# Optimization experiments

Hardware: AMD Instinct MI355X
Metric: run time of the kernel (lower is better)

## Reference

```python
import jax, jax.numpy as jnp
import numpy as np

MS_KS = 9
C = 256
BN_EPS = 1e-5


def setup_inputs() -> dict:
    key = jax.random.key(0)
    k1, k2, k3 = jax.random.split(key, 3)
    p2_r = jax.random.normal(k1, (2, C, 64, 128), dtype=jnp.float32)
    conv_w = jax.random.normal(k2, (C, C, 1, MS_KS), dtype=jnp.float32) * 0.02
    conv1_w = jax.random.normal(k3, (1, C, 1, 1), dtype=jnp.float32) * 0.05
    bn_gamma = jnp.ones((1,), jnp.float32)
    bn_beta = jnp.zeros((1,), jnp.float32)
    return dict(p2_r=p2_r, conv_w=conv_w, conv1_w=conv1_w,
                bn_gamma=bn_gamma, bn_beta=bn_beta)


def _scnn_pass(x, M):
    # x: [b,c,h,w]. Each step applies conv(1,ms_ks) to a width-1 column with
    # zero padding ms_ks//2 -> only the center tap contributes, i.e. a 256x256
    # channel matmul per column, followed by relu and residual add.
    cols = jnp.moveaxis(x, 3, 0)  # [w,b,c,h]
    def step(carry, col):
        new = col + jax.nn.relu(jnp.einsum('oc,bch->boh', M, carry))
        return new, new
    _, outs = jax.lax.scan(step, cols[0], cols[1:])
    outs = jnp.concatenate([cols[:1], outs], axis=0)[::-1]  # mirrors out[::-1]
    return jnp.moveaxis(outs, 0, 3)


def _upsample_bilinear_ac(x, factor=4):
    # F.interpolate(mode='bilinear', align_corners=True)
    b, c, h, w = x.shape
    Ho, Wo = factor * h, factor * w
    ys = jnp.arange(Ho, dtype=x.dtype) * ((h - 1) / (Ho - 1))
    xs = jnp.arange(Wo, dtype=x.dtype) * ((w - 1) / (Wo - 1))
    y0 = jnp.floor(ys).astype(jnp.int32)
    y1 = jnp.minimum(y0 + 1, h - 1)
    wy = (ys - y0.astype(x.dtype))[None, None, :, None]
    rows = x[:, :, y0, :] * (1 - wy) + x[:, :, y1, :] * wy  # [b,c,Ho,w]
    x0 = jnp.floor(xs).astype(jnp.int32)
    x1 = jnp.minimum(x0 + 1, w - 1)
    wx = (xs - x0.astype(x.dtype))[None, None, None, :]
    return rows[:, :, :, x0] * (1 - wx) + rows[:, :, :, x1] * wx


def reference(p2_r, conv_w, conv1_w, bn_gamma, bn_beta):
    M = conv_w[:, :, 0, MS_KS // 2]  # center tap, [c_out, c_in]
    x = _scnn_pass(p2_r, M)                     # reverse=False
    x = _scnn_pass(x[:, :, :, ::-1], M)         # reverse=True (slices[::-1])
    x = _upsample_bilinear_ac(x, 4)             # [b,256,4h,4w]
    x = jnp.einsum('oc,bchw->bohw', conv1_w[:, :, 0, 0], x)  # 1x1 conv -> 1 ch
    # BatchNorm2d(1), training-mode batch statistics (biased variance)
    mean = jnp.mean(x, axis=(0, 2, 3), keepdims=True)
    var = jnp.mean((x - mean) ** 2, axis=(0, 2, 3), keepdims=True)
    x = (x - mean) * jax.lax.rsqrt(var + BN_EPS)
    x = x * bn_gamma[None, :, None, None] + bn_beta[None, :, None, None]
    return jax.nn.sigmoid(x)
```

## Files before the change

kernel.cpp:

```cpp
#include <hip/hip_runtime.h>


typedef _Float16 f16x8 __attribute__((ext_vector_type(8)));
typedef _Float16 f16x4 __attribute__((ext_vector_type(4)));
typedef float    f32x4 __attribute__((ext_vector_type(4)));

static __device__ __forceinline__ void sync_lds() {
  asm volatile("s_waitcnt lgkmcnt(0)" ::: "memory");
  __builtin_amdgcn_s_barrier();
  asm volatile("" ::: "memory");
}

static __device__ __forceinline__ float dpp_even(float v) {
  int t = __builtin_bit_cast(int, v);
  t = __builtin_amdgcn_update_dpp(t, t, 0xA0, 0xF, 0xF, false);
  return __builtin_bit_cast(float, t);
}

extern "C" __global__ void k_extract(const float* __restrict__ convw,
                                     _Float16* __restrict__ Md) {
  int q = blockIdx.x * 256 + threadIdx.x;
  float4 v = ((const float4*)convw)[q];
  float vv[4] = {v.x, v.y, v.z, v.w};
  int f = q * 4;
#pragma unroll
  for (int e = 0; e < 4; ++e) {
    int flat = f + e;
    if (flat % 9 == 4) Md[flat / 9] = (_Float16)vv[e];
  }
}

struct SM {
  _Float16 cy[2][256];
  _Float16 pad_[32];
  _Float16 zh[128 * 256];
};

extern "C" __global__ void __launch_bounds__(512, 1)
k_scan(const float* __restrict__ p2, const _Float16* __restrict__ Md,
       const float* __restrict__ conv1, float* __restrict__ sout,
       float* __restrict__ stats) {
  __shared__ SM sm;
  const int tid  = threadIdx.x;
  const int l    = tid & 63;
  const int r    = tid >> 6;
  const int col  = l & 15;
  const int quad = l >> 4;
  const int b    = blockIdx.x >> 6;
  const int h    = blockIdx.x & 63;

  if (blockIdx.x == 0 && tid == 0) { stats[0] = 0.f; stats[1] = 0.f; }

  const bool isY   = (col == 0);
  const bool isZ   = (col == 1);
  const bool zlane = (l & 1);

  const int m0 = (r * 2 + 0) * 16 + quad * 4;
  const int m1 = (r * 2 + 1) * 16 + quad * 4;

  f16x8 A0[8], A1[8];
#pragma unroll
  for (int ch = 0; ch < 8; ++ch) {
    A0[ch] = *(const f16x8*)(Md + ((r*2+0)*16 + col) * 256 + ch*32 + quad*8);
    A1[ch] = *(const f16x8*)(Md + ((r*2+1)*16 + col) * 256 + ch*32 + quad*8);
  }

  const float* pbase = p2 + (size_t)b * 2097152 + (size_t)h * 128;

  float4 pA[4], pB[4], qA[4], qB[4];
  if (isY) {
#pragma unroll
    for (int i = 0; i < 4; ++i) {
      pA[i] = *(const float4*)(pbase + (size_t)(m0 + i) * 8192);
      pB[i] = *(const float4*)(pbase + (size_t)(m1 + i) * 8192);
      qA[i] = *(const float4*)(pbase + (size_t)(m0 + i) * 8192 + 4);
      qB[i] = *(const float4*)(pbase + (size_t)(m1 + i) * 8192 + 4);
    }
  }

  if (isY) {
    f16x4 pa, pb;
#pragma unroll
    for (int i = 0; i < 4; ++i) {
      pa[i] = (_Float16)pA[i].x; pb[i] = (_Float16)pB[i].x;
    }
    *(f16x4*)(sm.cy[0] + m0) = pa; *(f16x4*)(sm.cy[0] + m1) = pb;
    *(f16x4*)(sm.zh    + m0) = pa; *(f16x4*)(sm.zh    + m1) = pb;
  }
  sync_lds();

  const _Float16* pY0 = sm.cy[0] + quad * 8;
  const _Float16* pY1 = sm.cy[1] + quad * 8;
  const _Float16* zrd = sm.zh + quad * 8;
  _Float16*       zwr = sm.zh + 256;

#define STEP(PY, WY, CA, CB, COMP)                                             \
  do {                                                                         \
    const _Float16* bsrc = zlane ? zrd : (PY);                                 \
    f16x8 B[8];                                                                \
    _Pragma("unroll")                                                          \
    for (int ch = 0; ch < 8; ++ch)                                             \
      B[ch] = *(const f16x8*)(bsrc + ch * 32);                                 \
    f32x4 a00 = {0.f,0.f,0.f,0.f}, a01 = {0.f,0.f,0.f,0.f};                    \
    f32x4 a10 = {0.f,0.f,0.f,0.f}, a11 = {0.f,0.f,0.f,0.f};                    \
    _Pragma("unroll")                                                          \
    for (int ch = 0; ch < 4; ++ch) {                                           \
      a00 = __builtin_amdgcn_mfma_f32_16x16x32_f16(A0[ch],   B[ch],   a00,0,0,0);\
      a10 = __builtin_amdgcn_mfma_f32_16x16x32_f16(A1[ch],   B[ch],   a10,0,0,0);\
      a01 = __builtin_amdgcn_mfma_f32_16x16x32_f16(A0[ch+4], B[ch+4], a01,0,0,0);\
      a11 = __builtin_amdgcn_mfma_f32_16x16x32_f16(A1[ch+4], B[ch+4], a11,0,0,0);\
    }                                                                          \
    f32x4 acc0 = a00 + a01, acc1 = a10 + a11;                                  \
    f32x4 yf0 = {}, yf1 = {};                                                  \
    if (isY) {                                                                 \
      f16x4 yh0, yh1;                                                          \
      _Pragma("unroll")                                                        \
      for (int i = 0; i < 4; ++i) {                                            \
        yf0[i] = (CA)[i].COMP + fmaxf(acc0[i], 0.f);                           \
        yf1[i] = (CB)[i].COMP + fmaxf(acc1[i], 0.f);                           \
        yh0[i] = (_Float16)yf0[i]; yh1[i] = (_Float16)yf1[i];                  \
      }                                                                        \
      *(f16x4*)((WY) + m0) = yh0;                                              \
      *(f16x4*)((WY) + m1) = yh1;                                              \
    }                                                                          \
    _Pragma("unroll")                                                          \
    for (int i = 0; i < 4; ++i) {                                              \
      yf0[i] = dpp_even(yf0[i]);                                               \
      yf1[i] = dpp_even(yf1[i]);                                               \
    }                                                                          \
    if (isZ) {                                                                 \
      f16x4 zh0, zh1;                                                          \
      _Pragma("unroll")                                                        \
      for (int i = 0; i < 4; ++i) {                                            \
        zh0[i] = (_Float16)(yf0[i] + fmaxf(acc0[i], 0.f));                     \
        zh1[i] = (_Float16)(yf1[i] + fmaxf(acc1[i], 0.f));                     \
      }                                                                        \
      *(f16x4*)(zwr + m0) = zh0;                                               \
      *(f16x4*)(zwr + m1) = zh1;                                               \
    }                                                                          \
    zrd += 256; zwr += 256;                                                    \
    sync_lds();                                                                \
  } while (0)

#define REFILL(SA, SB, W0)                                                     \
  do {                                                                         \
    if (isY) {                                                                 \
      int wt = (W0) <= 124 ? (W0) : 124;                                       \
      _Pragma("unroll")                                                        \
      for (int i = 0; i < 4; ++i) {                                            \
        SA[i] = *(const float4*)(pbase + (size_t)(m0 + i) * 8192 + wt);        \
        SB[i] = *(const float4*)(pbase + (size_t)(m1 + i) * 8192 + wt);        \
      }                                                                        \
    }                                                                          \
  } while (0)

  STEP(pY0, sm.cy[1], pA, pB, y);
  STEP(pY1, sm.cy[0], pA, pB, z);
  STEP(pY0, sm.cy[1], pA, pB, w);
  REFILL(pA, pB, 8);

  int w0 = 4;
#pragma unroll 1
  for (int it = 0; it < 15; ++it) {
    STEP(pY1, sm.cy[0], qA, qB, x);
    STEP(pY0, sm.cy[1], qA, qB, y);
    STEP(pY1, sm.cy[0], qA, qB, z);
    STEP(pY0, sm.cy[1], qA, qB, w);
    REFILL(qA, qB, w0 + 8);
    STEP(pY1, sm.cy[0], pA, pB, x);
    STEP(pY0, sm.cy[1], pA, pB, y);
    STEP(pY1, sm.cy[0], pA, pB, z);
    STEP(pY0, sm.cy[1], pA, pB, w);
    REFILL(pA, pB, w0 + 12);
    w0 += 8;
  }

  STEP(pY1, sm.cy[0], qA, qB, x);
  STEP(pY0, sm.cy[1], qA, qB, y);
  STEP(pY1, sm.cy[0], qA, qB, z);
  STEP(pY0, sm.cy[1], qA, qB, w);
#undef STEP
#undef REFILL

  {
    const int w    = tid >> 2;
    const int part = tid & 3;
    const _Float16* zr = sm.zh + w * 256 + part * 64;
    const float*    vr = conv1 + part * 64;
    float s = 0.f;
#pragma unroll
    for (int j = 0; j < 8; ++j) {
      f16x8 zv = *(const f16x8*)(zr + j * 8);
      float4 v0 = *(const float4*)(vr + j * 8);
      float4 v1 = *(const float4*)(vr + j * 8 + 4);
      s += v0.x * (float)zv[0] + v0.y * (float)zv[1]
         + v0.z * (float)zv[2] + v0.w * (float)zv[3]
         + v1.x * (float)zv[4] + v1.y * (float)zv[5]
         + v1.z * (float)zv[6] + v1.w * (float)zv[7];
    }
    s += __shfl_xor(s, 1, 64);
    s += __shfl_xor(s, 2, 64);
    if (part == 0) sout[(blockIdx.x << 7) + (127 - w)] = s;
  }
}

static __device__ __forceinline__ float bilin(const float* __restrict__ s,
                                              int idx) {
  int bb  = idx >> 17;
  int rem = idx & 131071;
  int ho  = rem >> 9;
  int wo  = rem & 511;
  const float SY = 63.0f / 255.0f, SX = 127.0f / 511.0f;
  float fy = (float)ho * SY;
  int y0 = (int)fy; int y1 = min(y0 + 1, 63); float wy = fy - (float)y0;
  float fx = (float)wo * SX;
  int x0 = (int)fx; int x1 = min(x0 + 1, 127); float wx = fx - (float)x0;
  const float* sb = s + bb * 8192;
  float cA = sb[y0 * 128 + x0] * (1.f - wy) + sb[y1 * 128 + x0] * wy;
  float cB = sb[y0 * 128 + x1] * (1.f - wy) + sb[y1 * 128 + x1] * wy;
  return cA * (1.f - wx) + cB * wx;
}

extern "C" __global__ void k_stats(const float* __restrict__ s,
                                   float* __restrict__ stats) {
  int tid  = threadIdx.x;
  int base = blockIdx.x * 1024 + tid;
  float sum = 0.f, ssq = 0.f;
#pragma unroll
  for (int i = 0; i < 4; ++i) {
    float u = bilin(s, base + i * 256);
    sum += u; ssq += u * u;
  }
#pragma unroll
  for (int off = 32; off > 0; off >>= 1) {
    sum += __shfl_xor(sum, off, 64);
    ssq += __shfl_xor(ssq, off, 64);
  }
  __shared__ float ls[4], lq[4];
  int wv = tid >> 6;
  if ((tid & 63) == 0) { ls[wv] = sum; lq[wv] = ssq; }
  __syncthreads();
  if (tid == 0) {
    atomicAdd(&stats[0], ls[0] + ls[1] + ls[2] + ls[3]);
    atomicAdd(&stats[1], lq[0] + lq[1] + lq[2] + lq[3]);
  }
}

extern "C" __global__ void k_norm(const float* __restrict__ s,
                                  const float* __restrict__ stats,
                                  const float* __restrict__ gamma,
                                  const float* __restrict__ beta,
                                  float* __restrict__ out) {
  int tid  = threadIdx.x;
  int base = blockIdx.x * 1024 + tid;
  const float invN = 1.f / 262144.f;
  float mean  = stats[0] * invN;
  float var   = stats[1] * invN - mean * mean;
  float scale = rsqrtf(var + 1e-5f) * gamma[0];
  float bias  = beta[0] - mean * scale;
#pragma unroll
  for (int i = 0; i < 4; ++i) {
    int idx = base + i * 256;
    float u = bilin(s, idx);
    float x = u * scale + bias;
    out[idx] = 1.f / (1.f + __expf(-x));
  }
}

extern "C" void kernel_launch(void* const* d_in, const int* in_sizes, int n_in,
                              void* d_out, int out_size, void* d_ws, size_t ws_size,
                              hipStream_t stream) {
  const float* p2    = (const float*)d_in[0];
  const float* convw = (const float*)d_in[1];
  const float* conv1 = (const float*)d_in[2];
  const float* gamma = (const float*)d_in[3];
  const float* beta  = (const float*)d_in[4];
  float* out = (float*)d_out;

  char* ws = (char*)d_ws;
  float*    s     = (float*)ws;
  float*    stats = (float*)(ws + 65536);
  _Float16* Md    = (_Float16*)(ws + 65792);

  hipLaunchKernelGGL(k_extract, dim3(576), dim3(256), 0, stream, convw, Md);
  hipLaunchKernelGGL(k_scan,    dim3(128), dim3(512), 0, stream, p2, Md, conv1, s, stats);
  hipLaunchKernelGGL(k_stats,   dim3(256), dim3(256), 0, stream, s, stats);
  hipLaunchKernelGGL(k_norm,    dim3(256), dim3(256), 0, stream, s, stats, gamma, beta, out);
}
```

Measured before the change: 176.3 us.

## Compute BN statistics analytically from low-res map via bilinear weight moments

Replaces the per-output bilinear sum/sum-of-squares reduction with a closed-form computation. Per-axis bilinear weight moments are precomputed and combined with row sums, row self-products and adjacent-row cross-products of the 64x128 pre-upsample map, in a single block. This removes the atomics and the 256-block pass over the 262144 upsampled values. The cost is one serial single-block kernel whose threads loop over 128-wide rows, and float precision in var = E[x²]-mean² is unchanged. Normalisation scale and bias are now precomputed once for the norm kernel.

Result: no change. 179.1 us (+1.6%).

```diff
diff --git a/kernel.cpp b/kernel.cpp
--- a/kernel.cpp
+++ b/kernel.cpp
@@ -38,8 +38,7 @@
 
 extern "C" __global__ void __launch_bounds__(512, 1)
 k_scan(const float* __restrict__ p2, const _Float16* __restrict__ Md,
-       const float* __restrict__ conv1, float* __restrict__ sout,
-       float* __restrict__ stats) {
+       const float* __restrict__ conv1, float* __restrict__ sout) {
   __shared__ SM sm;
   const int tid  = threadIdx.x;
   const int l    = tid & 63;
@@ -48,8 +47,6 @@
   const int quad = l >> 4;
   const int b    = blockIdx.x >> 6;
   const int h    = blockIdx.x & 63;
-
-  if (blockIdx.x == 0 && tid == 0) { stats[0] = 0.f; stats[1] = 0.f; }
 
   const bool isY   = (col == 0);
   const bool isZ   = (col == 1);
@@ -222,42 +219,109 @@
 }
 
 extern "C" __global__ void k_stats(const float* __restrict__ s,
+                                   const float* __restrict__ gamma,
+                                   const float* __restrict__ beta,
                                    float* __restrict__ stats) {
-  int tid  = threadIdx.x;
-  int base = blockIdx.x * 1024 + tid;
-  float sum = 0.f, ssq = 0.f;
-#pragma unroll
-  for (int i = 0; i < 4; ++i) {
-    float u = bilin(s, base + i * 256);
-    sum += u; ssq += u * u;
+  __shared__ float CX[128], CXX[128], CXY[128];
+  __shared__ float CY[64],  DYY[64],  DYZ[64];
+  __shared__ float P[128], Rr[128], C2[126];
+  __shared__ float w1[4], w2[4];
+  const int tid = threadIdx.x;
+  const float SY = 63.0f / 255.0f, SX = 127.0f / 511.0f;
+
+  if (tid < 128) {
+    const int x = tid;
+    float cx = 0.f, cxx = 0.f, cxy = 0.f;
+    int lo = (x - 1) * 511 / 127 - 2; if (lo < 0) lo = 0;
+    int hi = (x + 1) * 511 / 127 + 2; if (hi > 511) hi = 511;
+    for (int wo = lo; wo <= hi; ++wo) {
+      float fx = (float)wo * SX;
+      int x0 = (int)fx; int x1 = min(x0 + 1, 127); float wx = fx - (float)x0;
+      if (x0 == x) {
+        float a = 1.f - wx;
+        cx += a; cxx += a * a;
+        if (x1 == x + 1) cxy += 2.f * a * wx;
+      }
+      if (x1 == x && x0 == x - 1) { cx += wx; cxx += wx * wx; }
+    }
+    CX[x] = cx; CXX[x] = cxx; CXY[x] = cxy;
+  } else if (tid < 192) {
+    const int y = tid - 128;
+    float cy = 0.f, dyy = 0.f, dyz = 0.f;
+    int lo = (y - 1) * 255 / 63 - 2; if (lo < 0) lo = 0;
+    int hi = (y + 1) * 255 / 63 + 2; if (hi > 255) hi = 255;
+    for (int ho = lo; ho <= hi; ++ho) {
+      float fy = (float)ho * SY;
+      int y0 = (int)fy; int y1 = min(y0 + 1, 63); float wy = fy - (float)y0;
+      if (y0 == y) {
+        float a = 1.f - wy;
+        cy += a; dyy += a * a;
+        if (y1 == y + 1) dyz += 2.f * a * wy;
+      }
+      if (y1 == y && y0 == y - 1) { cy += wy; dyy += wy * wy; }
+    }
+    CY[y] = cy; DYY[y] = dyy; DYZ[y] = dyz;
+  }
+  __syncthreads();
+
+  if (tid < 128) {
+    const float* row = s + (tid >> 6) * 8192 + (tid & 63) * 128;
+    float p = 0.f, rr = 0.f;
+    for (int x = 0; x < 127; ++x) {
+      p  += CXX[x] * row[x] * row[x] + CXY[x] * row[x] * row[x + 1];
+      rr += CX[x] * row[x];
+    }
+    p  += CXX[127] * row[127] * row[127];
+    rr += CX[127] * row[127];
+    P[tid] = p; Rr[tid] = rr;
+  } else if (tid < 254) {
+    const int k  = tid - 128;
+    const int bb = (k >= 63);
+    const int y  = k - 63 * bb;
+    const float* u = s + bb * 8192 + y * 128;
+    const float* v = u + 128;
+    float c = 0.f;
+    for (int x = 0; x < 127; ++x)
+      c += CXX[x] * u[x] * v[x]
+         + 0.5f * CXY[x] * (u[x] * v[x + 1] + u[x + 1] * v[x]);
+    c += CXX[127] * u[127] * v[127];
+    C2[k] = c;
+  }
+  __syncthreads();
+
+  float s1 = 0.f, s2 = 0.f;
+  if (tid < 128) {
+    const int bb = tid >> 6, y = tid & 63;
+    s1 = CY[y] * Rr[tid];
+    s2 = DYY[y] * P[tid];
+    if (y < 63) s2 += DYZ[y] * C2[bb * 63 + y];
   }
 #pragma unroll
   for (int off = 32; off > 0; off >>= 1) {
-    sum += __shfl_xor(sum, off, 64);
-    ssq += __shfl_xor(ssq, off, 64);
-  }
-  __shared__ float ls[4], lq[4];
-  int wv = tid >> 6;
-  if ((tid & 63) == 0) { ls[wv] = sum; lq[wv] = ssq; }
+    s1 += __shfl_xor(s1, off, 64);
+    s2 += __shfl_xor(s2, off, 64);
+  }
+  if ((tid & 63) == 0) { w1[tid >> 6] = s1; w2[tid >> 6] = s2; }
   __syncthreads();
   if (tid == 0) {
-    atomicAdd(&stats[0], ls[0] + ls[1] + ls[2] + ls[3]);
-    atomicAdd(&stats[1], lq[0] + lq[1] + lq[2] + lq[3]);
+    float S1 = w1[0] + w1[1] + w1[2] + w1[3];
+    float S2 = w2[0] + w2[1] + w2[2] + w2[3];
+    const float invN = 1.f / 262144.f;
+    float mean  = S1 * invN;
+    float var   = S2 * invN - mean * mean;
+    float scale = rsqrtf(var + 1e-5f) * gamma[0];
+    stats[0] = scale;
+    stats[1] = beta[0] - mean * scale;
   }
 }
 
 extern "C" __global__ void k_norm(const float* __restrict__ s,
                                   const float* __restrict__ stats,
-                                  const float* __restrict__ gamma,
-                                  const float* __restrict__ beta,
                                   float* __restrict__ out) {
   int tid  = threadIdx.x;
   int base = blockIdx.x * 1024 + tid;
-  const float invN = 1.f / 262144.f;
-  float mean  = stats[0] * invN;
-  float var   = stats[1] * invN - mean * mean;
-  float scale = rsqrtf(var + 1e-5f) * gamma[0];
-  float bias  = beta[0] - mean * scale;
+  float scale = stats[0];
+  float bias  = stats[1];
 #pragma unroll
   for (int i = 0; i < 4; ++i) {
     int idx = base + i * 256;
@@ -283,7 +347,7 @@
   _Float16* Md    = (_Float16*)(ws + 65792);
 
   hipLaunchKernelGGL(k_extract, dim3(576), dim3(256), 0, stream, convw, Md);
-  hipLaunchKernelGGL(k_scan,    dim3(128), dim3(512), 0, stream, p2, Md, conv1, s, stats);
-  hipLaunchKernelGGL(k_stats,   dim3(256), dim3(256), 0, stream, s, stats);
-  hipLaunchKernelGGL(k_norm,    dim3(256), dim3(256), 0, stream, s, stats, gamma, beta, out);
-}
+  hipLaunchKernelGGL(k_scan,    dim3(128), dim3(512), 0, stream, p2, Md, conv1, s);
+  hipLaunchKernelGGL(k_stats,   dim3(1),   dim3(256), 0, stream, s, gamma, beta, stats);
+  hipLaunchKernelGGL(k_norm,    dim3(256), dim3(256), 0, stream, s, stats, out);
+}
```
